# Kernel optimization log

Measured on AMD Instinct MI355X. Metric: run time of the kernel, lower is better.

The kernel has to match this reference:

```python
import jax, jax.numpy as jnp
import numpy as np

DIM = 192
HEADS = 8
EPS = 1e-12  # torch F.normalize eps


def setup_inputs() -> dict:
    key = jax.random.key(0)
    k1, k2, k3, k4 = jax.random.split(key, 4)
    b, c, h, w = 2, DIM, 256, 256
    x = jax.random.normal(k1, (b, c, h, w), dtype=jnp.float32)
    # 1x1 conv weights stored as (out, in)
    qkv_w = jax.random.normal(k2, (3 * c, c), dtype=jnp.float32) * (1.0 / np.sqrt(c))
    # depthwise 3x3, groups = 3c -> OIHW with I=1
    dw_w = jax.random.normal(k3, (3 * c, 1, 3, 3), dtype=jnp.float32) * (1.0 / 3.0)
    proj_w = jax.random.normal(k4, (c, c), dtype=jnp.float32) * (1.0 / np.sqrt(c))
    temperature = jnp.ones((HEADS, 1, 1), dtype=jnp.float32)
    return {"x": x, "qkv_w": qkv_w, "dw_w": dw_w, "proj_w": proj_w,
            "temperature": temperature}


def _l2norm(t):
    n = jnp.sqrt(jnp.sum(t * t, axis=-1, keepdims=True))
    return t / jnp.maximum(n, EPS)


def reference(x, qkv_w, dw_w, proj_w, temperature):
    b, c, h, w = x.shape
    # 1x1 conv (pointwise) -> depthwise 3x3 conv
    qkv = jnp.einsum('oc,bchw->bohw', qkv_w, x)  # (b, 3c, h, w)
    qkv = jax.lax.conv_general_dilated(
        qkv, dw_w, window_strides=(1, 1), padding='SAME',
        feature_group_count=3 * c,
        dimension_numbers=('NCHW', 'OIHW', 'NCHW'))
    q, k, v = jnp.split(qkv, 3, axis=1)
    # faithful reshape: full C channels per head, spatial dim split by heads
    q = q.reshape(b, HEADS, c, -1)
    k = k.reshape(b, HEADS, c, -1)
    v = v.reshape(b, HEADS, c, -1)
    q = _l2norm(q)
    k = _l2norm(k)
    attn = jnp.einsum('bhcn,bhdn->bhcd', q, k) * temperature  # (b,H,c,c)
    attn = jax.nn.softmax(attn, axis=-1)
    out = jnp.einsum('bhcd,bhdn->bhcn', attn, v)
    out = out.reshape(b, c, h, w)
    out = jnp.einsum('oc,bchw->bohw', proj_w, out)
    return out
```

## Files before the change

### kernel.cpp

```cpp
#include <hip/hip_runtime.h>
#include <math.h>

typedef unsigned short u16;
typedef unsigned int   u32;
typedef short bf16x8 __attribute__((ext_vector_type(8)));
typedef float f32x4  __attribute__((ext_vector_type(4)));

#define MFMA16(a,b,c) __builtin_amdgcn_mfma_f32_16x16x32_bf16((a),(b),(c),0,0,0)

__device__ __forceinline__ float bf2f(u16 h){ u32 u=((u32)h)<<16; return __uint_as_float(u); }
__device__ __forceinline__ u16 f2bf(float f){ u32 u=__float_as_uint(f); return (u16)((u+0x7fffu+((u>>16)&1u))>>16); }

__device__ __forceinline__ void gl2lds(const u16* g, u16* l){
  __builtin_amdgcn_global_load_lds((const __attribute__((address_space(1))) u32*)g,
                                   (__attribute__((address_space(3))) u32*)l, 16, 0, 0);
}
__device__ __forceinline__ void stc(u16* p, float v){ *p = f2bf(v); }
__device__ __forceinline__ void stc(float* p, float v){ *p = v; }
__device__ __forceinline__ void ld4(const float* p, float* v){ float4 x=*(const float4*)p; v[0]=x.x;v[1]=x.y;v[2]=x.z;v[3]=x.w; }
__device__ __forceinline__ void ld4(const u16* p, float* v){ ushort4 x=*(const ushort4*)p; v[0]=bf2f(x.x);v[1]=bf2f(x.y);v[2]=bf2f(x.z);v[3]=bf2f(x.w); }

__device__ __forceinline__ int xcd_remap(){
  int gx = gridDim.x, gy = gridDim.y;
  int lin = blockIdx.x + gx*(blockIdx.y + gy*blockIdx.z);
  int nwg = gx*gy*gridDim.z;
  if (nwg & 7) return lin;
  int q = nwg >> 3;
  return (lin & 7)*q + (lin >> 3);
}

__global__ void prep_kernel(const float* __restrict__ qkv_w, const float* __restrict__ proj_w,
                            u16* __restrict__ wq, u16* __restrict__ wp, float* __restrict__ norms){
  int i = blockIdx.x*256 + threadIdx.x;
  if (i < 110592) wq[i] = f2bf(qkv_w[i]);
  else if (i < 147456) wp[i-110592] = f2bf(proj_w[i-110592]);
  else if (i < 156672) norms[i-147456] = 0.f;
}

template<typename TIN>
__global__ __launch_bounds__(256) void transpose_kernel(
    const TIN* __restrict__ in, u16* __restrict__ out,
    long in_hi, long in_lo, long out_slab, int in_pitch)
{
  __shared__ float tile[64][65];
  const int t = threadIdx.x;
  const int z = blockIdx.z;
  const TIN* ip = in + (long)(z>>3)*in_hi + (long)(z&7)*in_lo;
  u16* op = out + (long)z*out_slab;
  const int s0 = blockIdx.x*64, c0 = blockIdx.y*64;
  const int rl = t>>4, cc = (t&15)*4;
#pragma unroll
  for (int rr=0; rr<4; rr++){
    int row = rr*16 + rl;
    float v[4];
    ld4(ip + (long)(c0+row)*in_pitch + s0 + cc, v);
    tile[row][cc+0]=v[0]; tile[row][cc+1]=v[1]; tile[row][cc+2]=v[2]; tile[row][cc+3]=v[3];
  }
  __syncthreads();
#pragma unroll
  for (int wr=0; wr<4; wr++){
    int sl = wr*16 + rl;
    ushort4 s;
    s.x = f2bf(tile[cc+0][sl]); s.y = f2bf(tile[cc+1][sl]);
    s.z = f2bf(tile[cc+2][sl]); s.w = f2bf(tile[cc+3][sl]);
    *(ushort4*)(op + (long)(s0+sl)*192 + c0 + cc) = s;
  }
}

template<typename TC>
__global__ __launch_bounds__(256) void gemm_nt_kernel(
    const u16* __restrict__ A, const u16* __restrict__ B, TC* __restrict__ C,
    int M, long sB, long sC)
{
  __shared__ __align__(16) u16 As[128*32];
  __shared__ __align__(16) u16 Bs[128*32];
  const int t = threadIdx.x, w = t>>6, l = t&63;
  const int wrk = xcd_remap();
  const int mt = wrk % gridDim.x;
  const int rest = wrk / gridDim.x;
  const int nt = rest % gridDim.y, bz = rest / gridDim.y;
  const int m0 = mt*128, n0 = nt*128;
  const u16* Bb = B + (long)bz*sB + (long)n0*192;
  const int rq = t>>2, qq = (t&3)*8;
  int ar0 = m0 + rq;      if (ar0 >= M) ar0 = M-1;
  int ar1 = m0 + 64 + rq; if (ar1 >= M) ar1 = M-1;
  f32x4 acc[4][4];
#pragma unroll
  for (int i=0;i<4;i++)
#pragma unroll
    for (int j=0;j<4;j++) acc[i][j] = f32x4{0.f,0.f,0.f,0.f};

  for (int k0=0; k0<192; k0+=32){
    __syncthreads();
    gl2lds(A + (long)ar0*192 + k0 + qq, As + t*8);
    gl2lds(A + (long)ar1*192 + k0 + qq, As + (256+t)*8);
    gl2lds(Bb + (long)rq*192 + k0 + qq, Bs + t*8);
    gl2lds(Bb + (long)(64+rq)*192 + k0 + qq, Bs + (256+t)*8);
    __syncthreads();
    const u16* ap = As + ((w>>1)*64 + (l&15))*32 + (l>>4)*8;
    const u16* bp = Bs + ((w&1)*64 + (l&15))*32 + (l>>4)*8;
    bf16x8 a[4], b[4];
#pragma unroll
    for (int i=0;i<4;i++){ a[i] = *(const bf16x8*)(ap + i*512); b[i] = *(const bf16x8*)(bp + i*512); }
#pragma unroll
    for (int i=0;i<4;i++)
#pragma unroll
      for (int j=0;j<4;j++) acc[i][j] = MFMA16(a[i], b[j], acc[i][j]);
  }
  const int mw = m0 + (w>>1)*64, nw = n0 + (w&1)*64;
  TC* Cb = C + (long)bz*sC;
#pragma unroll
  for (int i=0;i<4;i++){
#pragma unroll
    for (int r=0;r<4;r++){
      int row = mw + i*16 + (l>>4)*4 + r;
      if (row < M){
        TC* cp = Cb + (long)row*65536 + nw + (l&15);
#pragma unroll
        for (int j=0;j<4;j++) stc(cp + j*16, acc[i][j][r]);
      }
    }
  }
}

__global__ __launch_bounds__(256) void dwconv_kernel(
    const u16* __restrict__ in, const float* __restrict__ w9s,
    u16* __restrict__ out, float* __restrict__ norms)
{
  const int bo = blockIdx.x >> 4;
  const int rt = blockIdx.x & 15;
  const int o  = bo % 576;
  const u16* ip = in + (long)bo*65536L;
  u16* op = out + (long)bo*65536L;
  float w[9];
#pragma unroll
  for (int i=0;i<9;i++) w[i] = w9s[o*9+i];
  __shared__ float tile[18*264];
  const int t = threadIdx.x;
  if (t < 144){
    int row = t >> 3, c = t & 7;
    tile[row*264 + ((c<4) ? c : 256+c)] = 0.f;
  }
  for (int vi=t; vi<1152; vi+=256){
    int row = vi>>6, col = (vi&63)<<2;
    int g = rt*16 - 1 + row;
    float4 f;
    if (g >= 0 && g < 256){
      ushort4 u = *(const ushort4*)(ip + g*256 + col);
      f = make_float4(bf2f(u.x), bf2f(u.y), bf2f(u.z), bf2f(u.w));
    } else f = make_float4(0.f,0.f,0.f,0.f);
    *(float4*)&tile[row*264 + 4 + col] = f;
  }
  __syncthreads();
  const int tx = t & 63, ty = t >> 6;
  const float* base = &tile[4 + tx*4];
  float acc[4][4];
#pragma unroll
  for (int i=0;i<4;i++)
#pragma unroll
    for (int j=0;j<4;j++) acc[i][j] = 0.f;
#pragma unroll
  for (int r=0; r<6; r++){
    const float* row = base + (ty*4 + r)*264;
    float4 L = *(const float4*)(row - 4);
    float4 M = *(const float4*)(row);
    float4 R = *(const float4*)(row + 4);
    const float lf=L.w, m0=M.x, m1=M.y, m2=M.z, m3=M.w, rg=R.x;
#pragma unroll
    for (int ro=0; ro<4; ro++){
      if (r-ro >= 0 && r-ro <= 2){
        const int wr = (r-ro)*3;
        acc[ro][0] = fmaf(w[wr],lf, fmaf(w[wr+1],m0, fmaf(w[wr+2],m1, acc[ro][0])));
        acc[ro][1] = fmaf(w[wr],m0, fmaf(w[wr+1],m1, fmaf(w[wr+2],m2, acc[ro][1])));
        acc[ro][2] = fmaf(w[wr],m1, fmaf(w[wr+1],m2, fmaf(w[wr+2],m3, acc[ro][2])));
        acc[ro][3] = fmaf(w[wr],m2, fmaf(w[wr+1],m3, fmaf(w[wr+2],rg, acc[ro][3])));
      }
    }
  }
  float ss = 0.f;
#pragma unroll
  for (int ro=0; ro<4; ro++){
    ushort4 s;
    s.x = f2bf(acc[ro][0]); s.y = f2bf(acc[ro][1]);
    s.z = f2bf(acc[ro][2]); s.w = f2bf(acc[ro][3]);
    *(ushort4*)(op + (rt*16 + ty*4 + ro)*256 + tx*4) = s;
#pragma unroll
    for (int j=0;j<4;j++) ss = fmaf(acc[ro][j], acc[ro][j], ss);
  }
#pragma unroll
  for (int off=32; off>=1; off>>=1) ss += __shfl_xor(ss, off);
  __shared__ float red[4];
  if ((t&63)==0) red[t>>6] = ss;
  __syncthreads();
  if (t==0 && o < 384){
    atomicAdd(&norms[bo*8 + (rt>>1)], red[0]+red[1]+red[2]+red[3]);
  }
}

__global__ __launch_bounds__(256) void gemm_qk_kernel(
    const u16* __restrict__ conv, float* __restrict__ part)
{
  __shared__ __align__(16) u16 As[64*64];
  __shared__ __align__(16) u16 Bs[64*64];
  const int t = threadIdx.x, w = t>>6, l = t&63;
  const int wrk = xcd_remap();
  const int mt = wrk % 3;
  const int rest = wrk / 3;
  const int nt = rest % 3, z = rest / 3;
  const int bh = z>>3, sl = z&7;
  const int b = bh>>3, h = bh&7;
  const u16* Q  = conv + (long)b*37748736L + (long)h*1572864L;
  const u16* Kp = Q + 12582912L;
  const int m0 = mt*64, n0 = nt*64;
  const int rq = t>>3, qq = (t&7)*8;
  const long qo0 = (long)(m0+rq)*8192 + qq;
  const long qo1 = (long)(m0+32+rq)*8192 + qq;
  const long ko0 = (long)(n0+rq)*8192 + qq;
  const long ko1 = (long)(n0+32+rq)*8192 + qq;
  f32x4 acc[2][2];
#pragma unroll
  for (int i=0;i<2;i++)
#pragma unroll
    for (int j=0;j<2;j++) acc[i][j] = f32x4{0.f,0.f,0.f,0.f};
  const int kbeg = sl*1024;
  for (int k0=kbeg; k0<kbeg+1024; k0+=64){
    __syncthreads();
    gl2lds(Q  + qo0 + k0, As + t*8);
    gl2lds(Q  + qo1 + k0, As + (256+t)*8);
    gl2lds(Kp + ko0 + k0, Bs + t*8);
    gl2lds(Kp + ko1 + k0, Bs + (256+t)*8);
    __syncthreads();
    const u16* ap = As + ((w>>1)*32 + (l&15))*64 + (l>>4)*8;
    const u16* bp = Bs + ((w&1)*32 + (l&15))*64 + (l>>4)*8;
#pragma unroll
    for (int ks=0; ks<2; ks++){
      bf16x8 a0 = *(const bf16x8*)(ap + ks*32);
      bf16x8 a1 = *(const bf16x8*)(ap + 1024 + ks*32);
      bf16x8 b0 = *(const bf16x8*)(bp + ks*32);
      bf16x8 b1 = *(const bf16x8*)(bp + 1024 + ks*32);
      acc[0][0]=MFMA16(a0,b0,acc[0][0]); acc[0][1]=MFMA16(a0,b1,acc[0][1]);
      acc[1][0]=MFMA16(a1,b0,acc[1][0]); acc[1][1]=MFMA16(a1,b1,acc[1][1]);
    }
  }
  float* P = part + (long)z*36864L;
  const int mw = m0 + (w>>1)*32, nw = n0 + (w&1)*32;
#pragma unroll
  for (int i=0;i<2;i++)
#pragma unroll
    for (int j=0;j<2;j++)
#pragma unroll
      for (int r=0;r<4;r++)
        P[(long)(mw + i*16 + (l>>4)*4 + r)*192 + nw + j*16 + (l&15)] = acc[i][j][r];
}

__global__ __launch_bounds__(64) void softmax_kernel(
    const float* __restrict__ part, const float* __restrict__ temp,
    const float* __restrict__ norms, u16* __restrict__ attn)
{
  const int rg = blockIdx.x;
  const int bh = rg/192, r = rg - bh*192;
  const int b = bh>>3, h = bh&7;
  const int t = threadIdx.x;
  const float tp = temp[h];
  const float sq = norms[(b*576 + 24*h + (r>>3))*8 + (r&7)];
  const float invq = 1.f/fmaxf(sqrtf(sq), 1e-12f);
  const float* P = part + (long)bh*8L*36864L + (long)r*192;
  float lv[3];
#pragma unroll
  for (int j=0;j<3;j++){
    int col = t + j*64;
    float s = 0.f;
#pragma unroll
    for (int ks=0; ks<8; ks++) s += P[(long)ks*36864L + col];
    float sk = norms[(b*576 + 192 + 24*h + (col>>3))*8 + (col&7)];
    float invk = 1.f/fmaxf(sqrtf(sk), 1e-12f);
    lv[j] = s*invq*invk*tp;
  }
  float mx = fmaxf(lv[0], fmaxf(lv[1], lv[2]));
#pragma unroll
  for (int o=32;o>=1;o>>=1) mx = fmaxf(mx, __shfl_xor(mx, o));
  float e[3], sum = 0.f;
#pragma unroll
  for (int j=0;j<3;j++){ e[j] = expf(lv[j]-mx); sum += e[j]; }
#pragma unroll
  for (int o=32;o>=1;o>>=1) sum += __shfl_xor(sum, o);
  const float inv = 1.f/sum;
  u16* ap = attn + (long)bh*36864L + (long)r*192;
#pragma unroll
  for (int j=0;j<3;j++) ap[t + j*64] = f2bf(e[j]*inv);
}

__global__ __launch_bounds__(256) void gemm_av_kernel(
    const u16* __restrict__ VT, const u16* __restrict__ attn, u16* __restrict__ out_sc)
{
  __shared__ __align__(16) char smem[69632];
  u16* As = (u16*)smem;
  u16* Bs = (u16*)(smem + 8192);
  const int t = threadIdx.x, w = t>>6, l = t&63;
  const int wrk = xcd_remap();
  const int mt = wrk % 64;
  const int rest = wrk / 64;
  const int nt = rest % 2, bh = rest / 2;
  const int b = bh>>3, h = bh&7;
  const u16* Av = VT + (long)bh*1572864L;
  const u16* Bt = attn + (long)bh*36864L;
  const int m0 = mt*128, n0 = nt*128;
  const int rq = t>>2, qq = (t&3)*8;
  int br0 = n0 + rq;      if (br0 > 191) br0 = 191;
  int br1 = n0 + 64 + rq; if (br1 > 191) br1 = 191;
  f32x4 acc[4][4];
#pragma unroll
  for (int i=0;i<4;i++)
#pragma unroll
    for (int j=0;j<4;j++) acc[i][j] = f32x4{0.f,0.f,0.f,0.f};
  for (int k0=0; k0<192; k0+=32){
    __syncthreads();
    gl2lds(Av + (long)(m0+rq)*192 + k0 + qq, As + t*8);
    gl2lds(Av + (long)(m0+64+rq)*192 + k0 + qq, As + (256+t)*8);
    gl2lds(Bt + (long)br0*192 + k0 + qq, Bs + t*8);
    gl2lds(Bt + (long)br1*192 + k0 + qq, Bs + (256+t)*8);
    __syncthreads();
    const u16* ap = As + ((w>>1)*64 + (l&15))*32 + (l>>4)*8;
    const u16* bp = Bs + ((w&1)*64 + (l&15))*32 + (l>>4)*8;
    bf16x8 a[4], bb[4];
#pragma unroll
    for (int i=0;i<4;i++){ a[i] = *(const bf16x8*)(ap + i*512); bb[i] = *(const bf16x8*)(bp + i*512); }
#pragma unroll
    for (int i=0;i<4;i++)
#pragma unroll
      for (int j=0;j<4;j++) acc[i][j] = MFMA16(a[i], bb[j], acc[i][j]);
  }
  __syncthreads();
  float* wb = (float*)smem + w*4352;
#pragma unroll
  for (int i=0;i<4;i++)
#pragma unroll
    for (int j=0;j<4;j++)
#pragma unroll
      for (int r=0;r<4;r++)
        wb[(i*16 + (l>>4)*4 + r)*68 + j*16 + (l&15)] = acc[i][j][r];
  __syncthreads();
  const int c0w = nt*128 + (w&1)*64;
  if (c0w < 192){
    const int cb = 24*h + (c0w>>3);
    const int mw = m0 + (w>>1)*64;
    u16* ob = out_sc + (long)b*12582912L + cb;
    const int nl0 = l>>3, sb = l&7;
#pragma unroll
    for (int ri=0; ri<8; ri++){
      int nl = ri*8 + nl0;
      const float* src = wb + nl*68 + sb;
      u32 d0 = (u32)f2bf(src[0])  | ((u32)f2bf(src[8])  << 16);
      u32 d1 = (u32)f2bf(src[16]) | ((u32)f2bf(src[24]) << 16);
      u32 d2 = (u32)f2bf(src[32]) | ((u32)f2bf(src[40]) << 16);
      u32 d3 = (u32)f2bf(src[48]) | ((u32)f2bf(src[56]) << 16);
      *(uint4*)(ob + ((long)sb*8192 + mw + nl)*192) = make_uint4(d0,d1,d2,d3);
    }
  }
}

extern "C" void kernel_launch(void* const* d_in, const int* in_sizes, int n_in,
                              void* d_out, int out_size, void* d_ws, size_t ws_size,
                              hipStream_t stream)
{
  const float* x      = (const float*)d_in[0];
  const float* qkv_w  = (const float*)d_in[1];
  const float* dw_w   = (const float*)d_in[2];
  const float* proj_w = (const float*)d_in[3];
  const float* temp   = (const float*)d_in[4];
  float* out = (float*)d_out;

  char* ws = (char*)d_ws;
  u16*   xT      = (u16*)(ws + 0);
  u16*   conv    = (u16*)(ws + 0);
  u16*   qkv_raw = (u16*)(ws + 150994944);
  u16*   VT      = (u16*)(ws + 150994944);
  u16*   out_sc  = (u16*)(ws + 201326592);
  float* part    = (float*)(ws + 251658240);
  u16*   attn    = (u16*)(ws + 270532608);
  u16*   wq_bf   = (u16*)(ws + 301989888);
  u16*   wp_bf   = (u16*)(ws + 302211072);
  float* norms   = (float*)(ws + 302284800);

  prep_kernel<<<dim3(612), 256, 0, stream>>>(qkv_w, proj_w, wq_bf, wp_bf, norms);

  transpose_kernel<float><<<dim3(1024, 3, 2), 256, 0, stream>>>(
      x, xT, 0L, 12582912L, 12582912L, 65536);

  gemm_nt_kernel<u16><<<dim3(5, 512, 2), 256, 0, stream>>>(
      wq_bf, xT, qkv_raw, 576, 12582912L, 37748736L);

  dwconv_kernel<<<dim3(1152*16), 256, 0, stream>>>(qkv_raw, dw_w, conv, norms);

  transpose_kernel<u16><<<dim3(128, 3, 16), 256, 0, stream>>>(
      conv + 25165824L, VT, 37748736L, 1572864L, 1572864L, 8192);

  gemm_qk_kernel<<<dim3(3, 3, 128), 256, 0, stream>>>(conv, part);

  softmax_kernel<<<dim3(3072), 64, 0, stream>>>(part, temp, norms, attn);

  gemm_av_kernel<<<dim3(64, 2, 16), 256, 0, stream>>>(VT, attn, out_sc);

  gemm_nt_kernel<float><<<dim3(2, 512, 2), 256, 0, stream>>>(
      wp_bf, out_sc, out, 192, 12582912L, 12582912L);
}
```

Baseline: 451.5 us.

## Stream depthwise conv rows through registers with wave shuffles instead of LDS tiles

The depthwise 3x3 conv no longer stages an 18-row fp32 tile in LDS. Each wavefront now walks 16 output rows (18 input rows) top to bottom, keeps three rolling row accumulators in registers, and gets left and right neighbours through cross-lane shuffles. This removes the LDS traffic, the halo reloads and the block barrier, and cuts the grid to a quarter of the blocks. The cost is one atomicAdd per wave for the norms, and the loads become serial within a wave, so less parallelism is available to hide memory latency. Separately, the softmax kernel now packs four rows per 256-thread block instead of one row per 64-thread block.

```diff
diff --git a/kernel.cpp b/kernel.cpp
--- a/kernel.cpp
+++ b/kernel.cpp
@@ -127,73 +127,57 @@
     const u16* __restrict__ in, const float* __restrict__ w9s,
     u16* __restrict__ out, float* __restrict__ norms)
 {
-  const int bo = blockIdx.x >> 4;
-  const int rt = blockIdx.x & 15;
+  const int bo = blockIdx.x >> 2;
+  const int rg = blockIdx.x & 3;
   const int o  = bo % 576;
-  const u16* ip = in + (long)bo*65536L;
-  u16* op = out + (long)bo*65536L;
+  const int t = threadIdx.x, wv = t>>6, l = t&63;
+  const u16* ip = in + (long)bo*65536L + l*4;
+  u16* op = out + (long)bo*65536L + l*4;
   float w[9];
 #pragma unroll
   for (int i=0;i<9;i++) w[i] = w9s[o*9+i];
-  __shared__ float tile[18*264];
-  const int t = threadIdx.x;
-  if (t < 144){
-    int row = t >> 3, c = t & 7;
-    tile[row*264 + ((c<4) ? c : 256+c)] = 0.f;
-  }
-  for (int vi=t; vi<1152; vi+=256){
-    int row = vi>>6, col = (vi&63)<<2;
-    int g = rt*16 - 1 + row;
-    float4 f;
-    if (g >= 0 && g < 256){
-      ushort4 u = *(const ushort4*)(ip + g*256 + col);
-      f = make_float4(bf2f(u.x), bf2f(u.y), bf2f(u.z), bf2f(u.w));
-    } else f = make_float4(0.f,0.f,0.f,0.f);
-    *(float4*)&tile[row*264 + 4 + col] = f;
-  }
-  __syncthreads();
-  const int tx = t & 63, ty = t >> 6;
-  const float* base = &tile[4 + tx*4];
-  float acc[4][4];
-#pragma unroll
-  for (int i=0;i<4;i++)
-#pragma unroll
-    for (int j=0;j<4;j++) acc[i][j] = 0.f;
-#pragma unroll
-  for (int r=0; r<6; r++){
-    const float* row = base + (ty*4 + r)*264;
-    float4 L = *(const float4*)(row - 4);
-    float4 M = *(const float4*)(row);
-    float4 R = *(const float4*)(row + 4);
-    const float lf=L.w, m0=M.x, m1=M.y, m2=M.z, m3=M.w, rg=R.x;
-#pragma unroll
-    for (int ro=0; ro<4; ro++){
-      if (r-ro >= 0 && r-ro <= 2){
-        const int wr = (r-ro)*3;
-        acc[ro][0] = fmaf(w[wr],lf, fmaf(w[wr+1],m0, fmaf(w[wr+2],m1, acc[ro][0])));
-        acc[ro][1] = fmaf(w[wr],m0, fmaf(w[wr+1],m1, fmaf(w[wr+2],m2, acc[ro][1])));
-        acc[ro][2] = fmaf(w[wr],m1, fmaf(w[wr+1],m2, fmaf(w[wr+2],m3, acc[ro][2])));
-        acc[ro][3] = fmaf(w[wr],m2, fmaf(w[wr+1],m3, fmaf(w[wr+2],rg, acc[ro][3])));
-      }
+  const int r0 = rg*64 + wv*16;
+  float ap0=0.f,ap1=0.f,ap2=0.f,ap3=0.f;
+  float ac0=0.f,ac1=0.f,ac2=0.f,ac3=0.f;
+  float an0,an1,an2,an3;
+  float ss = 0.f;
+#pragma unroll
+  for (int it=0; it<18; ++it){
+    const int g = r0 - 1 + it;
+    float v0,v1,v2,v3;
+    if (g>=0 && g<256){
+      ushort4 u = *(const ushort4*)(ip + g*256);
+      v0=bf2f(u.x); v1=bf2f(u.y); v2=bf2f(u.z); v3=bf2f(u.w);
+    } else { v0=0.f; v1=0.f; v2=0.f; v3=0.f; }
+    float sl = __shfl(v3, (l+63)&63);
+    float sr = __shfl(v0, (l+1)&63);
+    const float lf  = (l==0)  ? 0.f : sl;
+    const float rgt = (l==63) ? 0.f : sr;
+    ap0 = fmaf(w[6],lf, fmaf(w[7],v0, fmaf(w[8],v1, ap0)));
+    ap1 = fmaf(w[6],v0, fmaf(w[7],v1, fmaf(w[8],v2, ap1)));
+    ap2 = fmaf(w[6],v1, fmaf(w[7],v2, fmaf(w[8],v3, ap2)));
+    ap3 = fmaf(w[6],v2, fmaf(w[7],v3, fmaf(w[8],rgt, ap3)));
+    if (it >= 2){
+      ushort4 s;
+      s.x = f2bf(ap0); s.y = f2bf(ap1); s.z = f2bf(ap2); s.w = f2bf(ap3);
+      *(ushort4*)(op + (g-1)*256) = s;
+      ss = fmaf(ap0,ap0, fmaf(ap1,ap1, fmaf(ap2,ap2, fmaf(ap3,ap3, ss))));
     }
-  }
-  float ss = 0.f;
-#pragma unroll
-  for (int ro=0; ro<4; ro++){
-    ushort4 s;
-    s.x = f2bf(acc[ro][0]); s.y = f2bf(acc[ro][1]);
-    s.z = f2bf(acc[ro][2]); s.w = f2bf(acc[ro][3]);
-    *(ushort4*)(op + (rt*16 + ty*4 + ro)*256 + tx*4) = s;
-#pragma unroll
-    for (int j=0;j<4;j++) ss = fmaf(acc[ro][j], acc[ro][j], ss);
+    ac0 = fmaf(w[3],lf, fmaf(w[4],v0, fmaf(w[5],v1, ac0)));
+    ac1 = fmaf(w[3],v0, fmaf(w[4],v1, fmaf(w[5],v2, ac1)));
+    ac2 = fmaf(w[3],v1, fmaf(w[4],v2, fmaf(w[5],v3, ac2)));
+    ac3 = fmaf(w[3],v2, fmaf(w[4],v3, fmaf(w[5],rgt, ac3)));
+    an0 = fmaf(w[0],lf, fmaf(w[1],v0, w[2]*v1));
+    an1 = fmaf(w[0],v0, fmaf(w[1],v1, w[2]*v2));
+    an2 = fmaf(w[0],v1, fmaf(w[1],v2, w[2]*v3));
+    an3 = fmaf(w[0],v2, fmaf(w[1],v3, w[2]*rgt));
+    ap0=ac0; ap1=ac1; ap2=ac2; ap3=ac3;
+    ac0=an0; ac1=an1; ac2=an2; ac3=an3;
   }
 #pragma unroll
   for (int off=32; off>=1; off>>=1) ss += __shfl_xor(ss, off);
-  __shared__ float red[4];
-  if ((t&63)==0) red[t>>6] = ss;
-  __syncthreads();
-  if (t==0 && o < 384){
-    atomicAdd(&norms[bo*8 + (rt>>1)], red[0]+red[1]+red[2]+red[3]);
+  if (o < 384 && l == 0){
+    atomicAdd(&norms[bo*8 + (r0>>5)], ss);
   }
 }
 
@@ -253,14 +237,14 @@
         P[(long)(mw + i*16 + (l>>4)*4 + r)*192 + nw + j*16 + (l&15)] = acc[i][j][r];
 }
 
-__global__ __launch_bounds__(64) void softmax_kernel(
+__global__ __launch_bounds__(256) void softmax_kernel(
     const float* __restrict__ part, const float* __restrict__ temp,
     const float* __restrict__ norms, u16* __restrict__ attn)
 {
-  const int rg = blockIdx.x;
+  const int t = threadIdx.x, wv = t>>6, l = t&63;
+  const int rg = blockIdx.x*4 + wv;
   const int bh = rg/192, r = rg - bh*192;
   const int b = bh>>3, h = bh&7;
-  const int t = threadIdx.x;
   const float tp = temp[h];
   const float sq = norms[(b*576 + 24*h + (r>>3))*8 + (r&7)];
   const float invq = 1.f/fmaxf(sqrtf(sq), 1e-12f);
@@ -268,7 +252,7 @@
   float lv[3];
 #pragma unroll
   for (int j=0;j<3;j++){
-    int col = t + j*64;
+    int col = l + j*64;
     float s = 0.f;
 #pragma unroll
     for (int ks=0; ks<8; ks++) s += P[(long)ks*36864L + col];
@@ -287,7 +271,7 @@
   const float inv = 1.f/sum;
   u16* ap = attn + (long)bh*36864L + (long)r*192;
 #pragma unroll
-  for (int j=0;j<3;j++) ap[t + j*64] = f2bf(e[j]*inv);
+  for (int j=0;j<3;j++) ap[l + j*64] = f2bf(e[j]*inv);
 }
 
 __global__ __launch_bounds__(256) void gemm_av_kernel(
@@ -390,14 +374,14 @@
   gemm_nt_kernel<u16><<<dim3(5, 512, 2), 256, 0, stream>>>(
       wq_bf, xT, qkv_raw, 576, 12582912L, 37748736L);
 
-  dwconv_kernel<<<dim3(1152*16), 256, 0, stream>>>(qkv_raw, dw_w, conv, norms);
+  dwconv_kernel<<<dim3(1152*4), 256, 0, stream>>>(qkv_raw, dw_w, conv, norms);
 
   transpose_kernel<u16><<<dim3(128, 3, 16), 256, 0, stream>>>(
       conv + 25165824L, VT, 37748736L, 1572864L, 1572864L, 8192);
 
   gemm_qk_kernel<<<dim3(3, 3, 128), 256, 0, stream>>>(conv, part);
 
-  softmax_kernel<<<dim3(3072), 64, 0, stream>>>(part, temp, norms, attn);
+  softmax_kernel<<<dim3(768), 256, 0, stream>>>(part, temp, norms, attn);
 
   gemm_av_kernel<<<dim3(64, 2, 16), 256, 0, stream>>>(VT, attn, out_sc);
 
```

Result: slower. 464.0 us (+2.8%).
